# Performance work log

Hardware: AMD Instinct MI355X
Metric: run time of the kernel (lower is better)

## Reference

```python
import jax, jax.numpy as jnp
import numpy as np

CUTOFF = 5.0
N = 8192
BOX = 55.0


def setup_inputs() -> dict:
    key = jax.random.key(0)
    xyz = jax.random.uniform(key, (N, 3), dtype=jnp.float32) * BOX
    cell = jnp.diag(jnp.full((3,), BOX, dtype=jnp.float32))  # [3,3] box vectors (rows)
    ii, jj = np.triu_indices(N, k=1)  # all i<j candidate pairs, P = N*(N-1)/2
    return {
        "xyz": xyz,
        "cell": cell,
        "idx_i": jnp.asarray(ii, dtype=jnp.int32),
        "idx_j": jnp.asarray(jj, dtype=jnp.int32),
    }


def _min_image_deltas(xyz, cell, idx_i, idx_j):
    # [P,3] raw displacement for every candidate pair
    delta = xyz[idx_i] - xyz[idx_j]
    # triclinic minimum-image reduction, z -> y -> x order (NNPOps convention)
    delta = delta - jnp.round(delta[:, 2:3] / cell[2, 2]) * cell[2]
    delta = delta - jnp.round(delta[:, 1:2] / cell[1, 1]) * cell[1]
    delta = delta - jnp.round(delta[:, 0:1] / cell[0, 0]) * cell[0]
    dist = jnp.sqrt(jnp.sum(delta * delta, axis=1))  # [P]
    return delta, dist


def reference(xyz, cell, idx_i, idx_j):
    delta, dist = _min_image_deltas(xyz, cell, idx_i, idx_j)
    mask = dist < CUTOFF  # [P] bool
    # neighbors: -1 marks pairs beyond cutoff (fixed-shape output, jit-safe)
    pair_i = jnp.where(mask, idx_i, jnp.int32(-1))
    pair_j = jnp.where(mask, idx_j, jnp.int32(-1))
    pair_diff = jnp.where(mask[:, None], delta, jnp.float32(0.0))  # [P,3]
    pair_dist = jnp.where(mask, dist, jnp.float32(0.0))  # [P]
    return pair_i, pair_j, pair_diff, pair_dist
```

## Files before the change

kernel.cpp:

```cpp
#include <hip/hip_runtime.h>
#include <math.h>


#define NL_CUTOFF 5.0f

__device__ __forceinline__ void solve_ij(int p, int N, int& io, int& jo) {
    const int A = 2 * N - 1;
    const int disc = A * A - 8 * p;
    const float sd = __fsqrt_rn((float)disc);
    int ii = (int)(__fmul_rn(__fsub_rn((float)A, sd), 0.5f));
    if (ii < 0) ii = 0;
    if (ii > N - 2) ii = N - 2;
    while (ii > 0 && ((ii * (A - ii)) >> 1) > p) --ii;
    while ((((ii + 1) * (A - ii - 1)) >> 1) <= p) ++ii;
    io = ii;
    jo = p - ((ii * (A - ii)) >> 1) + ii + 1;
}

struct CellC {
    float r0x, r0y, r0z, rc0;
    float r1x, r1y, r1z, rc1;
    float r2x, r2y, r2z, rc2;
};

template <bool DIAG>
__device__ __forceinline__ void pair_compute(
    float xi, float yi, float zi, float xj, float yj, float zj,
    const CellC& c,
    float& odx, float& ody, float& odz, float& orr, bool& om)
{
    float dx = __fsub_rn(xi, xj);
    float dy = __fsub_rn(yi, yj);
    float dz = __fsub_rn(zi, zj);

    if (DIAG) {
        float s = rintf(__fmul_rn(dz, c.rc2));
        dz = __fsub_rn(dz, __fmul_rn(s, c.r2z));
        s = rintf(__fmul_rn(dy, c.rc1));
        dy = __fsub_rn(dy, __fmul_rn(s, c.r1y));
        s = rintf(__fmul_rn(dx, c.rc0));
        dx = __fsub_rn(dx, __fmul_rn(s, c.r0x));
    } else {
        float s = rintf(__fmul_rn(dz, c.rc2));
        dx = __fsub_rn(dx, __fmul_rn(s, c.r2x));
        dy = __fsub_rn(dy, __fmul_rn(s, c.r2y));
        dz = __fsub_rn(dz, __fmul_rn(s, c.r2z));

        s = rintf(__fmul_rn(dy, c.rc1));
        dx = __fsub_rn(dx, __fmul_rn(s, c.r1x));
        dy = __fsub_rn(dy, __fmul_rn(s, c.r1y));
        dz = __fsub_rn(dz, __fmul_rn(s, c.r1z));

        s = rintf(__fmul_rn(dx, c.rc0));
        dx = __fsub_rn(dx, __fmul_rn(s, c.r0x));
        dy = __fsub_rn(dy, __fmul_rn(s, c.r0y));
        dz = __fsub_rn(dz, __fmul_rn(s, c.r0z));
    }

    float ss = __fadd_rn(__fadd_rn(__fmul_rn(dx, dx), __fmul_rn(dy, dy)),
                         __fmul_rn(dz, dz));
    float r = __fsqrt_rn(ss);
    om  = (r < NL_CUTOFF);
    odx = dx;
    ody = dy;
    odz = dz;
    orr = r;
}

template <bool DIAG>
__device__ __forceinline__ void nl_body(
    const float* __restrict__ xyz, const CellC& c,
    float* __restrict__ out, long long P, int N)
{
    float* __restrict__ out_i = out;
    float* __restrict__ out_j = out + P;
    float* __restrict__ out_d = out + 2 * P;
    float* __restrict__ out_r = out + 5 * P;

    const long long nquad  = P >> 2;
    const long long stride = (long long)gridDim.x * blockDim.x;
    const long long tid0   = (long long)blockIdx.x * blockDim.x + threadIdx.x;

    for (long long q = tid0; q < nquad; q += stride) {
        int i, j;
        solve_ij((int)(q << 2), N, i, j);

        float dxa[4], dya[4], dza[4], ra[4];
        bool  ma[4];
        float oia[4], oja[4];
        if (j + 3 <= N - 1) {
            const float xi = xyz[3 * i + 0], yi = xyz[3 * i + 1], zi = xyz[3 * i + 2];
            const float fi = (float)i, fj = (float)j;
#pragma unroll
            for (int k = 0; k < 4; ++k) {
                pair_compute<DIAG>(xi, yi, zi,
                                   xyz[3 * (j + k) + 0], xyz[3 * (j + k) + 1],
                                   xyz[3 * (j + k) + 2],
                                   c, dxa[k], dya[k], dza[k], ra[k], ma[k]);
                oia[k] = ma[k] ? fi : -1.0f;
                oja[k] = ma[k] ? fj + (float)k : -1.0f;
            }
        } else {
            int ii = i, jj = j;
#pragma unroll
            for (int k = 0; k < 4; ++k) {
                pair_compute<DIAG>(xyz[3 * ii + 0], xyz[3 * ii + 1], xyz[3 * ii + 2],
                                   xyz[3 * jj + 0], xyz[3 * jj + 1], xyz[3 * jj + 2],
                                   c, dxa[k], dya[k], dza[k], ra[k], ma[k]);
                oia[k] = ma[k] ? (float)ii : -1.0f;
                oja[k] = ma[k] ? (float)jj : -1.0f;
                if (++jj >= N) { ++ii; jj = ii + 1; }
            }
        }

        ((float4*)out_i)[q] = make_float4(oia[0], oia[1], oia[2], oia[3]);
        ((float4*)out_j)[q] = make_float4(oja[0], oja[1], oja[2], oja[3]);

        if (ma[0] | ma[1] | ma[2] | ma[3]) {
#pragma unroll
            for (int k = 0; k < 4; ++k) {
                if (ma[k]) {
                    const long long p = (q << 2) + k;
                    out_d[3 * p + 0] = dxa[k];
                    out_d[3 * p + 1] = dya[k];
                    out_d[3 * p + 2] = dza[k];
                    out_r[p]         = ra[k];
                }
            }
        }
    }

    for (long long p = (nquad << 2) + tid0; p < P; p += stride) {
        int i, j;
        solve_ij((int)p, N, i, j);
        float dx, dy, dz, rr;
        bool  m;
        pair_compute<DIAG>(xyz[3 * i + 0], xyz[3 * i + 1], xyz[3 * i + 2],
                           xyz[3 * j + 0], xyz[3 * j + 1], xyz[3 * j + 2],
                           c, dx, dy, dz, rr, m);
        out_i[p] = m ? (float)i : -1.0f;
        out_j[p] = m ? (float)j : -1.0f;
        if (m) {
            out_d[3 * p + 0] = dx;
            out_d[3 * p + 1] = dy;
            out_d[3 * p + 2] = dz;
            out_r[p]         = rr;
        }
    }
}

__global__ __launch_bounds__(256) void nl_kernel(
    const float* __restrict__ xyz,
    const float* __restrict__ cell,
    float* __restrict__ out,
    long long P, int N)
{
    CellC c;
    c.r0x = cell[0]; c.r0y = cell[1]; c.r0z = cell[2];
    c.r1x = cell[3]; c.r1y = cell[4]; c.r1z = cell[5];
    c.r2x = cell[6]; c.r2y = cell[7]; c.r2z = cell[8];
    c.rc0 = __fdiv_rn(1.0f, c.r0x);
    c.rc1 = __fdiv_rn(1.0f, c.r1y);
    c.rc2 = __fdiv_rn(1.0f, c.r2z);

    const bool diag = (c.r0y == 0.0f) && (c.r0z == 0.0f) &&
                      (c.r1x == 0.0f) && (c.r1z == 0.0f) &&
                      (c.r2x == 0.0f) && (c.r2y == 0.0f);

    if (diag) nl_body<true>(xyz, c, out, P, N);
    else      nl_body<false>(xyz, c, out, P, N);
}

extern "C" void kernel_launch(void* const* d_in, const int* in_sizes, int n_in,
                              void* d_out, int out_size, void* d_ws, size_t ws_size,
                              hipStream_t stream) {
    const float* xyz  = (const float*)d_in[0];
    const float* cell = (const float*)d_in[1];
    float* out = (float*)d_out;

    const int       N = in_sizes[0] / 3;
    const long long P = (long long)in_sizes[2];

    hipMemsetAsync(out + 2 * P, 0, (size_t)(4 * P) * sizeof(float), stream);

    const int block = 256;
    long long nquad = P >> 2;
    long long blocks_needed = (nquad + block - 1) / block;
    int grid = (int)(blocks_needed < 2048 ? (blocks_needed > 0 ? blocks_needed : 1)
                                          : 2048);

    nl_kernel<<<grid, block, 0, stream>>>(xyz, cell, out, P, N);
}
```

Baseline: 190.4 us.

## Drop memset and 4-wide batching; write all outputs per pair directly

Removes the separate memset that zeroed the diff and dist outputs. Each thread now handles one pair and writes every output field itself, with zeros where the pair is masked out. The four-pairs-per-thread path with float4 stores to the index arrays is gone, index arithmetic drops from 64-bit to 32-bit, and launch bounds now ask for 8 blocks per CU. The memset pass and the kernel's partial writes are replaced by a single full write per output, at the cost of scalar rather than vectorised index stores and a sqrt-based index solve on every pair instead of every fourth.

```diff
diff --git a/kernel.cpp b/kernel.cpp
--- a/kernel.cpp
+++ b/kernel.cpp
@@ -70,90 +70,41 @@
 template <bool DIAG>
 __device__ __forceinline__ void nl_body(
     const float* __restrict__ xyz, const CellC& c,
-    float* __restrict__ out, long long P, int N)
+    float* __restrict__ out, int P, int N)
 {
     float* __restrict__ out_i = out;
     float* __restrict__ out_j = out + P;
-    float* __restrict__ out_d = out + 2 * P;
-    float* __restrict__ out_r = out + 5 * P;
+    float* __restrict__ out_d = out + 2 * (long long)P;
+    float* __restrict__ out_r = out + 5 * (long long)P;
 
-    const long long nquad  = P >> 2;
-    const long long stride = (long long)gridDim.x * blockDim.x;
-    const long long tid0   = (long long)blockIdx.x * blockDim.x + threadIdx.x;
+    const int stride = (int)(gridDim.x * blockDim.x);
+    const int tid0   = (int)(blockIdx.x * blockDim.x + threadIdx.x);
 
-    for (long long q = tid0; q < nquad; q += stride) {
+    for (int p = tid0; p < P; p += stride) {
         int i, j;
-        solve_ij((int)(q << 2), N, i, j);
+        solve_ij(p, N, i, j);
 
-        float dxa[4], dya[4], dza[4], ra[4];
-        bool  ma[4];
-        float oia[4], oja[4];
-        if (j + 3 <= N - 1) {
-            const float xi = xyz[3 * i + 0], yi = xyz[3 * i + 1], zi = xyz[3 * i + 2];
-            const float fi = (float)i, fj = (float)j;
-#pragma unroll
-            for (int k = 0; k < 4; ++k) {
-                pair_compute<DIAG>(xi, yi, zi,
-                                   xyz[3 * (j + k) + 0], xyz[3 * (j + k) + 1],
-                                   xyz[3 * (j + k) + 2],
-                                   c, dxa[k], dya[k], dza[k], ra[k], ma[k]);
-                oia[k] = ma[k] ? fi : -1.0f;
-                oja[k] = ma[k] ? fj + (float)k : -1.0f;
-            }
-        } else {
-            int ii = i, jj = j;
-#pragma unroll
-            for (int k = 0; k < 4; ++k) {
-                pair_compute<DIAG>(xyz[3 * ii + 0], xyz[3 * ii + 1], xyz[3 * ii + 2],
-                                   xyz[3 * jj + 0], xyz[3 * jj + 1], xyz[3 * jj + 2],
-                                   c, dxa[k], dya[k], dza[k], ra[k], ma[k]);
-                oia[k] = ma[k] ? (float)ii : -1.0f;
-                oja[k] = ma[k] ? (float)jj : -1.0f;
-                if (++jj >= N) { ++ii; jj = ii + 1; }
-            }
-        }
+        const float xi = xyz[3 * i + 0], yi = xyz[3 * i + 1], zi = xyz[3 * i + 2];
+        const float xj = xyz[3 * j + 0], yj = xyz[3 * j + 1], zj = xyz[3 * j + 2];
 
-        ((float4*)out_i)[q] = make_float4(oia[0], oia[1], oia[2], oia[3]);
-        ((float4*)out_j)[q] = make_float4(oja[0], oja[1], oja[2], oja[3]);
-
-        if (ma[0] | ma[1] | ma[2] | ma[3]) {
-#pragma unroll
-            for (int k = 0; k < 4; ++k) {
-                if (ma[k]) {
-                    const long long p = (q << 2) + k;
-                    out_d[3 * p + 0] = dxa[k];
-                    out_d[3 * p + 1] = dya[k];
-                    out_d[3 * p + 2] = dza[k];
-                    out_r[p]         = ra[k];
-                }
-            }
-        }
-    }
-
-    for (long long p = (nquad << 2) + tid0; p < P; p += stride) {
-        int i, j;
-        solve_ij((int)p, N, i, j);
         float dx, dy, dz, rr;
         bool  m;
-        pair_compute<DIAG>(xyz[3 * i + 0], xyz[3 * i + 1], xyz[3 * i + 2],
-                           xyz[3 * j + 0], xyz[3 * j + 1], xyz[3 * j + 2],
-                           c, dx, dy, dz, rr, m);
+        pair_compute<DIAG>(xi, yi, zi, xj, yj, zj, c, dx, dy, dz, rr, m);
+
         out_i[p] = m ? (float)i : -1.0f;
         out_j[p] = m ? (float)j : -1.0f;
-        if (m) {
-            out_d[3 * p + 0] = dx;
-            out_d[3 * p + 1] = dy;
-            out_d[3 * p + 2] = dz;
-            out_r[p]         = rr;
-        }
+        out_r[p] = m ? rr : 0.0f;
+        out_d[3 * p + 0] = m ? dx : 0.0f;
+        out_d[3 * p + 1] = m ? dy : 0.0f;
+        out_d[3 * p + 2] = m ? dz : 0.0f;
     }
 }
 
-__global__ __launch_bounds__(256) void nl_kernel(
+__global__ __launch_bounds__(256, 8) void nl_kernel(
     const float* __restrict__ xyz,
     const float* __restrict__ cell,
     float* __restrict__ out,
-    long long P, int N)
+    int P, int N)
 {
     CellC c;
     c.r0x = cell[0]; c.r0y = cell[1]; c.r0z = cell[2];
@@ -178,14 +129,11 @@
     const float* cell = (const float*)d_in[1];
     float* out = (float*)d_out;
 
-    const int       N = in_sizes[0] / 3;
-    const long long P = (long long)in_sizes[2];
-
-    hipMemsetAsync(out + 2 * P, 0, (size_t)(4 * P) * sizeof(float), stream);
+    const int N = in_sizes[0] / 3;
+    const int P = in_sizes[2];
 
     const int block = 256;
-    long long nquad = P >> 2;
-    long long blocks_needed = (nquad + block - 1) / block;
+    long long blocks_needed = ((long long)P + block - 1) / block;
     int grid = (int)(blocks_needed < 2048 ? (blocks_needed > 0 ? blocks_needed : 1)
                                           : 2048);
 
```

After: 165.7 us. -13.0%, faster.
